# Kernel tuning notes

Hardware: AMD Instinct MI355X
Metric: run time of the kernel (lower is better)

## Reference

```python
import jax, jax.numpy as jnp
import numpy as np

B, S, E = 2, 4096, 1024
QD, VD = 64, 64
WIN, DIL = 5, 2


def setup_inputs() -> dict:
    key = jax.random.key(0)
    ks = jax.random.split(key, 7)
    sc = E ** -0.5  # linear-layer init scale
    return {
        "x": jax.random.normal(ks[0], (B, S, E), jnp.float32),
        "Wq": jax.random.normal(ks[1], (E, QD), jnp.float32) * sc,
        "bq": jnp.zeros((QD,), jnp.float32),
        "Wk": jax.random.normal(ks[2], (E, QD), jnp.float32) * sc,
        "bk": jnp.zeros((QD,), jnp.float32),
        "Wv": jax.random.normal(ks[3], (E, VD), jnp.float32) * sc,
        "bv": jnp.zeros((VD,), jnp.float32),
    }


def reference(x, Wq, bq, Wk, bk, Wv, bv):
    b, s, _ = x.shape
    Q = x @ Wq + bq  # (b, s, QD)
    K = x @ Wk + bk  # (b, s, QD)
    V = x @ Wv + bv  # (b, s, VD)

    half = WIN // 2
    offsets = DIL * (jnp.arange(WIN) - half)
    i = jnp.arange(s)                                  # (s,)
    j = i[None, :] + offsets[:, None]
    valid = (j >= 0) & (j < s)                         # in-range band entries
    jc = jnp.clip(j, 0, s - 1)

    Kg = K[:, jc, :]
    # per-offset diagonal dot products Q_i . K_{i+d}
    c = jnp.einsum('bsd,bwsd->bws', Q, Kg) * valid

    ib = jnp.broadcast_to(i[None, :], (WIN, s))
    # Banded score matrix, zeros off-band (as in the original: torch.zeros scatter).
    # Masked (invalid) entries add 0, so clipped index collisions are harmless.
    scores = jnp.zeros((b, s, s), x.dtype).at[:, ib, jc].add(c)

    attn = jax.nn.softmax(scores, axis=2)              # softmax over full row incl. zeros
    return attn @ V                                    # (b, s, VD)
```

## Files before the change

### kernel.cpp

```cpp
#include <hip/hip_runtime.h>
#include <hip/hip_bf16.h>

typedef __hip_bfloat16 bf16;
typedef short bf16x8 __attribute__((ext_vector_type(8)));
typedef float f32x4 __attribute__((ext_vector_type(4)));

#define S_LEN 4096
#define NBATCH 2
#define EDIM 1024
#define DDIM 64
#define MROWS (NBATCH * S_LEN)

union frag_u { bf16x8 v; bf16 e[8]; };

__device__ __forceinline__ void cvt_split(const float4& a, const float4& b,
                                          bf16x8& hi, bf16x8& lo) {
  float v[8] = {a.x, a.y, a.z, a.w, b.x, b.y, b.z, b.w};
  frag_u h, l;
#pragma unroll
  for (int e = 0; e < 8; e++) {
    bf16 hh = __float2bfloat16(v[e]);
    h.e[e] = hh;
    l.e[e] = __float2bfloat16(v[e] - __bfloat162float(hh));
  }
  hi = h.v;
  lo = l.v;
}

__global__ __launch_bounds__(256) void pack_w_kernel(
    const float* __restrict__ Wq, const float* __restrict__ Wk,
    const float* __restrict__ Wv, bf16* __restrict__ Wt2_hi,
    bf16* __restrict__ Wt2_lo, float* __restrict__ Vsum) {
  __shared__ float tile[64 * 65];
  const int mat = blockIdx.x >> 4;
  const int kb = blockIdx.x & 15;
  const int t = threadIdx.x;
  if (blockIdx.x == 0 && t < NBATCH * DDIM) Vsum[t] = 0.f;
  const float* W = (mat == 0) ? Wq : ((mat == 1) ? Wk : Wv);

#pragma unroll
  for (int i = 0; i < 4; i++) {
    int F = (i * 256 + t) * 4;
    int k = F >> 6;
    int n4 = F & 63;
    float4 v = *(const float4*)(const void*)(W + (size_t)(kb * 64 + k) * 64 + n4);
    tile[(n4 + 0) * 65 + k] = v.x;
    tile[(n4 + 1) * 65 + k] = v.y;
    tile[(n4 + 2) * 65 + k] = v.z;
    tile[(n4 + 3) * 65 + k] = v.w;
  }
  __syncthreads();

#pragma unroll
  for (int it = 0; it < 2; it++) {
    int uidx = it * 256 + t;
    int nl = uidx >> 3;
    int j_half = (uidx >> 2) & 1;
    int pp_k = uidx & 3;
    int ng = mat * 64 + nl;
    int n2 = ng >> 1;
    int sp = ((ng & 1) * 4 + pp_k) ^ (n2 & 7);
    int unit = n2 * 8 + sp;
    int j = kb * 2 + j_half;
    frag_u h, l;
#pragma unroll
    for (int e = 0; e < 8; e++) {
      float v = tile[nl * 65 + j_half * 32 + pp_k * 8 + e];
      bf16 hh = __float2bfloat16(v);
      h.e[e] = hh;
      l.e[e] = __float2bfloat16(v - __bfloat162float(hh));
    }
    size_t ob = (size_t)j * 6144 + unit * 8;
    *(bf16x8*)(void*)(Wt2_hi + ob) = h.v;
    *(bf16x8*)(void*)(Wt2_lo + ob) = l.v;
  }
}

__global__ __launch_bounds__(512, 2) void qkv_gemm_kernel(
    const float* __restrict__ x, const bf16* __restrict__ Wt2_hi,
    const bf16* __restrict__ Wt2_lo, const float* __restrict__ bq,
    const float* __restrict__ bk, const float* __restrict__ bv,
    float* __restrict__ qkv, float* __restrict__ Vsum) {
  __shared__ f32x4 red[4][64][6];
  const int tid = threadIdx.x;
  const int lane = tid & 63;
  const int wave = tid >> 6;
  const int nh = wave & 3;
  const int kh = wave >> 2;
  const int quad = lane >> 4;
  const int l16 = lane & 15;
  const int rowBase = blockIdx.x * 32;

  const int sp = ((l16 & 1) * 4 + quad) ^ ((l16 >> 1) & 7);
  const int loff = ((l16 >> 1) * 8 + sp) * 8;
  const bf16* bhp = Wt2_hi + (size_t)kh * 98304 + nh * 1536 + loff;
  const bf16* blp = Wt2_lo + (size_t)kh * 98304 + nh * 1536 + loff;

  const char* aB0 = (const char*)x + (size_t)(rowBase + l16) * 4096 +
                    kh * 2048 + quad * 32;
  const char* aB1 = aB0 + 16 * 4096;

  float4 Ab[5][2][2];
  bf16x8 Bh[3][3], Bl[3][3];
  f32x4 acc[2][3];
#pragma unroll
  for (int f = 0; f < 2; f++)
#pragma unroll
    for (int t = 0; t < 3; t++) acc[f][t] = (f32x4){0.f, 0.f, 0.f, 0.f};

#define LOADB(s, r)                                                          \
  {                                                                          \
    const bf16* _h = bhp + (size_t)(r) * 6144;                               \
    const bf16* _l = blp + (size_t)(r) * 6144;                               \
    Bh[s][0] = *(const bf16x8*)(const void*)(_h);                            \
    Bh[s][1] = *(const bf16x8*)(const void*)(_h + 512);                      \
    Bh[s][2] = *(const bf16x8*)(const void*)(_h + 1024);                     \
    Bl[s][0] = *(const bf16x8*)(const void*)(_l);                            \
    Bl[s][1] = *(const bf16x8*)(const void*)(_l + 512);                      \
    Bl[s][2] = *(const bf16x8*)(const void*)(_l + 1024);                     \
  }
#define LOADA(s, r)                                                          \
  {                                                                          \
    Ab[s][0][0] = *(const float4*)(const void*)(aB0 + (r) * 128);            \
    Ab[s][0][1] = *(const float4*)(const void*)(aB0 + (r) * 128 + 16);       \
    Ab[s][1][0] = *(const float4*)(const void*)(aB1 + (r) * 128);            \
    Ab[s][1][1] = *(const float4*)(const void*)(aB1 + (r) * 128 + 16);       \
  }

  LOADB(0, 0);
  LOADA(0, 0);
  LOADB(1, 1);
  LOADA(1, 1);
  LOADB(2, 2);
  LOADA(2, 2);
  LOADA(3, 3);
  LOADA(4, 4);
  asm volatile("" ::: "memory");

#pragma unroll
  for (int r = 0; r < 16; ++r) {
    bf16x8 ah0, al0, ah1, al1;
    cvt_split(Ab[r % 5][0][0], Ab[r % 5][0][1], ah0, al0);
    cvt_split(Ab[r % 5][1][0], Ab[r % 5][1][1], ah1, al1);
    const int s = r % 3;
#pragma unroll
    for (int t = 0; t < 3; t++) {
      acc[0][t] =
          __builtin_amdgcn_mfma_f32_16x16x32_bf16(ah0, Bh[s][t], acc[0][t], 0, 0, 0);
      acc[0][t] =
          __builtin_amdgcn_mfma_f32_16x16x32_bf16(ah0, Bl[s][t], acc[0][t], 0, 0, 0);
      acc[0][t] =
          __builtin_amdgcn_mfma_f32_16x16x32_bf16(al0, Bh[s][t], acc[0][t], 0, 0, 0);
      acc[1][t] =
          __builtin_amdgcn_mfma_f32_16x16x32_bf16(ah1, Bh[s][t], acc[1][t], 0, 0, 0);
      acc[1][t] =
          __builtin_amdgcn_mfma_f32_16x16x32_bf16(ah1, Bl[s][t], acc[1][t], 0, 0, 0);
      acc[1][t] =
          __builtin_amdgcn_mfma_f32_16x16x32_bf16(al1, Bh[s][t], acc[1][t], 0, 0, 0);
    }
    if (r + 3 < 16) LOADB((r + 3) % 3, r + 3);
    if (r + 5 < 16) LOADA((r + 5) % 5, r + 5);
    asm volatile("" ::: "memory");
  }
#undef LOADA
#undef LOADB

  if (kh == 1) {
#pragma unroll
    for (int f = 0; f < 2; f++)
#pragma unroll
      for (int t = 0; t < 3; t++) red[nh][lane][f * 3 + t] = acc[f][t];
  }
  __syncthreads();
  if (kh == 1) return;
#pragma unroll
  for (int f = 0; f < 2; f++)
#pragma unroll
    for (int t = 0; t < 3; t++) acc[f][t] += red[nh][lane][f * 3 + t];

  const int bb = rowBase >> 12;
#pragma unroll
  for (int f = 0; f < 2; f++)
#pragma unroll
    for (int t = 0; t < 3; t++) {
      int nt = nh * 3 + t;
      int n = nt * 16 + l16;
      int mat = n >> 6;
      int col = n & 63;
      float bias = (mat == 0) ? bq[col] : ((mat == 1) ? bk[col] : bv[col]);
      float* dst = qkv + (size_t)mat * MROWS * DDIM +
                   (size_t)(rowBase + f * 16 + quad * 4) * DDIM + col;
      float vs = 0.f;
#pragma unroll
      for (int rr = 0; rr < 4; rr++) {
        float val = acc[f][t][rr] + bias;
        dst[rr * DDIM] = val;
        vs += val;
      }
      if (nt >= 8) {
        vs += __shfl_xor(vs, 16, 64);
        vs += __shfl_xor(vs, 32, 64);
        if (quad == 0) atomicAdd(&Vsum[bb * DDIM + (n - 128)], vs);
      }
    }
}

__global__ __launch_bounds__(256) void attn_kernel(
    const float* __restrict__ qkv, const float* __restrict__ Vsum,
    float* __restrict__ out) {
  const float* Qf = qkv;
  const float* Kf = qkv + (size_t)MROWS * DDIM;
  const float* Vf = qkv + (size_t)2 * MROWS * DDIM;
  int l = threadIdx.x & 31;
  int qidx = blockIdx.x * 8 + (threadIdx.x >> 5);
  int b = qidx >> 12;
  int i = qidx & 4095;

  float2 q = *(const float2*)(const void*)(Qf + (size_t)qidx * DDIM + 2 * l);
  float sc[5];
  float2 vv[5];
  bool val[5];
#pragma unroll
  for (int w = 0; w < 5; w++) {
    int j = i + 2 * w - 4;
    val[w] = (j >= 0) && (j < S_LEN);
    int jj = val[w] ? j : i;
    size_t off = (size_t)(b * S_LEN + jj) * DDIM + 2 * l;
    float2 kk = *(const float2*)(const void*)(Kf + off);
    vv[w] = *(const float2*)(const void*)(Vf + off);
    float p = q.x * kk.x + q.y * kk.y;
#pragma unroll
    for (int d = 1; d < 32; d <<= 1) p += __shfl_xor(p, d, 64);
    sc[w] = p;
  }

  float mx = 0.f;
#pragma unroll
  for (int w = 0; w < 5; w++)
    if (val[w]) mx = fmaxf(mx, sc[w]);

  float denom = 0.f;
  float2 accv = {0.f, 0.f}, vsel = {0.f, 0.f};
  int nval = 0;
#pragma unroll
  for (int w = 0; w < 5; w++)
    if (val[w]) {
      float pexp = __expf(sc[w] - mx);
      denom += pexp;
      accv.x += pexp * vv[w].x;
      accv.y += pexp * vv[w].y;
      vsel.x += vv[w].x;
      vsel.y += vv[w].y;
      nval++;
    }
  float pbg = __expf(-mx);
  denom += pbg * (float)(S_LEN - nval);
  float2 vsm = *(const float2*)(const void*)(Vsum + b * DDIM + 2 * l);
  accv.x += pbg * (vsm.x - vsel.x);
  accv.y += pbg * (vsm.y - vsel.y);

  float2 o = {accv.x / denom, accv.y / denom};
  *(float2*)(void*)(out + (size_t)qidx * DDIM + 2 * l) = o;
}

extern "C" void kernel_launch(void* const* d_in, const int* in_sizes, int n_in,
                              void* d_out, int out_size, void* d_ws,
                              size_t ws_size, hipStream_t stream) {
  const float* x = (const float*)d_in[0];
  const float* Wq = (const float*)d_in[1];
  const float* bq = (const float*)d_in[2];
  const float* Wk = (const float*)d_in[3];
  const float* bk = (const float*)d_in[4];
  const float* Wv = (const float*)d_in[5];
  const float* bv = (const float*)d_in[6];
  float* out = (float*)d_out;

  char* ws = (char*)d_ws;
  bf16* Wt2_hi = (bf16*)ws;
  bf16* Wt2_lo = (bf16*)(ws + 393216);
  float* qkv = (float*)(ws + 786432);
  float* Vsum = (float*)(ws + 786432 + 6291456);

  hipLaunchKernelGGL(pack_w_kernel, dim3(48), dim3(256), 0, stream, Wq, Wk, Wv,
                     Wt2_hi, Wt2_lo, Vsum);
  hipLaunchKernelGGL(qkv_gemm_kernel, dim3(256), dim3(512), 0, stream, x,
                     Wt2_hi, Wt2_lo, bq, bk, bv, qkv, Vsum);
  hipLaunchKernelGGL(attn_kernel, dim3(1024), dim3(256), 0, stream, qkv, Vsum,
                     out);
}
```

Measured before the change: 113.4 us.

## Stage x tile into LDS with async global_load_lds before QKV GEMM

Replaces the per-thread register-prefetched float4 loads of x with a bulk asynchronous global-to-LDS copy of the block's whole 32x1024 fp32 tile, using an XOR swizzle, then reads A fragments from LDS inside the MFMA loop. The aim is coalesced wide loads and fewer VGPRs held for the A prefetch ring. In exchange it uses 128 KB of LDS per block, which conflicts with the launch bound of 2 blocks per CU and lowers occupancy. It also waits on the whole tile up front instead of pipelining it, and reuses the LDS buffer for the reduction after an added barrier.

Result: faster. 106.4 us (-6.2%).

```diff
diff --git a/kernel.cpp b/kernel.cpp
--- a/kernel.cpp
+++ b/kernel.cpp
@@ -11,7 +11,15 @@
 #define DDIM 64
 #define MROWS (NBATCH * S_LEN)
 
+#define GLOBAL_AS __attribute__((address_space(1)))
+#define LDS_AS __attribute__((address_space(3)))
+
 union frag_u { bf16x8 v; bf16 e[8]; };
+
+__device__ __forceinline__ void async_ld16(const void* gp, void* lp) {
+  __builtin_amdgcn_global_load_lds((const GLOBAL_AS void*)gp,
+                                   (LDS_AS void*)lp, 16, 0, 0);
+}
 
 __device__ __forceinline__ void cvt_split(const float4& a, const float4& b,
                                           bf16x8& hi, bf16x8& lo) {
@@ -81,7 +89,7 @@
     const bf16* __restrict__ Wt2_lo, const float* __restrict__ bq,
     const float* __restrict__ bk, const float* __restrict__ bv,
     float* __restrict__ qkv, float* __restrict__ Vsum) {
-  __shared__ f32x4 red[4][64][6];
+  __shared__ __align__(16) char lds[131072];
   const int tid = threadIdx.x;
   const int lane = tid & 63;
   const int wave = tid >> 6;
@@ -96,11 +104,6 @@
   const bf16* bhp = Wt2_hi + (size_t)kh * 98304 + nh * 1536 + loff;
   const bf16* blp = Wt2_lo + (size_t)kh * 98304 + nh * 1536 + loff;
 
-  const char* aB0 = (const char*)x + (size_t)(rowBase + l16) * 4096 +
-                    kh * 2048 + quad * 32;
-  const char* aB1 = aB0 + 16 * 4096;
-
-  float4 Ab[5][2][2];
   bf16x8 Bh[3][3], Bl[3][3];
   f32x4 acc[2][3];
 #pragma unroll
@@ -119,29 +122,37 @@
     Bl[s][1] = *(const bf16x8*)(const void*)(_l + 512);                      \
     Bl[s][2] = *(const bf16x8*)(const void*)(_l + 1024);                     \
   }
-#define LOADA(s, r)                                                          \
-  {                                                                          \
-    Ab[s][0][0] = *(const float4*)(const void*)(aB0 + (r) * 128);            \
-    Ab[s][0][1] = *(const float4*)(const void*)(aB0 + (r) * 128 + 16);       \
-    Ab[s][1][0] = *(const float4*)(const void*)(aB1 + (r) * 128);            \
-    Ab[s][1][1] = *(const float4*)(const void*)(aB1 + (r) * 128 + 16);       \
-  }
-
+
+#pragma unroll
+  for (int i = 0; i < 16; i++) {
+    const int Rl = (wave << 2) | (i >> 2);
+    const int g = i & 3;
+    const char* src = (const char*)x + (size_t)(rowBase + Rl) * 4096 +
+                      (size_t)g * 1024 + ((lane ^ (Rl & 7)) << 4);
+    async_ld16(src, lds + Rl * 4096 + g * 1024);
+  }
+  asm volatile("" ::: "memory");
   LOADB(0, 0);
-  LOADA(0, 0);
   LOADB(1, 1);
-  LOADA(1, 1);
   LOADB(2, 2);
-  LOADA(2, 2);
-  LOADA(3, 3);
-  LOADA(4, 4);
-  asm volatile("" ::: "memory");
+  asm volatile("s_waitcnt vmcnt(18)" ::: "memory");
+  __builtin_amdgcn_s_barrier();
+  __builtin_amdgcn_sched_barrier(0);
+
+  const char* aRow0 = lds + l16 * 4096;
+  const char* aRow1 = lds + (16 + l16) * 4096;
+  const int aE = (((quad * 2) ^ (l16 & 7)) << 4);
 
 #pragma unroll
   for (int r = 0; r < 16; ++r) {
+    const int Rk = kh * 16 + r;
+    float4 a00 = *(const float4*)(const void*)(aRow0 + Rk * 128 + aE);
+    float4 a01 = *(const float4*)(const void*)(aRow0 + Rk * 128 + (aE ^ 16));
+    float4 a10 = *(const float4*)(const void*)(aRow1 + Rk * 128 + aE);
+    float4 a11 = *(const float4*)(const void*)(aRow1 + Rk * 128 + (aE ^ 16));
     bf16x8 ah0, al0, ah1, al1;
-    cvt_split(Ab[r % 5][0][0], Ab[r % 5][0][1], ah0, al0);
-    cvt_split(Ab[r % 5][1][0], Ab[r % 5][1][1], ah1, al1);
+    cvt_split(a00, a01, ah0, al0);
+    cvt_split(a10, a11, ah1, al1);
     const int s = r % 3;
 #pragma unroll
     for (int t = 0; t < 3; t++) {
@@ -159,12 +170,12 @@
           __builtin_amdgcn_mfma_f32_16x16x32_bf16(al1, Bh[s][t], acc[1][t], 0, 0, 0);
     }
     if (r + 3 < 16) LOADB((r + 3) % 3, r + 3);
-    if (r + 5 < 16) LOADA((r + 5) % 5, r + 5);
     asm volatile("" ::: "memory");
   }
-#undef LOADA
 #undef LOADB
 
+  f32x4(*red)[64][6] = (f32x4(*)[64][6])lds;
+  __syncthreads();
   if (kh == 1) {
 #pragma unroll
     for (int f = 0; f < 2; f++)
```
